# Performance work log

Measured on AMD Instinct MI355X. Metric: run time of the kernel, lower is better.

The kernel has to match this reference:

```python
import jax, jax.numpy as jnp
import numpy as np

D_MODEL = 1024
H = 16
D_K = D_MODEL // H
B = 2
S = 2048
NEG = -1000000000.0


def setup_inputs() -> dict:
    key = jax.random.key(0)
    ks = jax.random.split(key, 11)
    sc = 1.0 / np.sqrt(D_MODEL)
    inp = {
        "q": jax.random.normal(ks[0], (B, S, D_MODEL), jnp.float32),
        "k": jax.random.normal(ks[1], (B, S, D_MODEL), jnp.float32),
        "v": jax.random.normal(ks[2], (B, S, D_MODEL), jnp.float32),
        "mask": jnp.tril(jnp.ones((S, S), jnp.int32))[None, None, :, :],  # causal [1,1,S,S]
        "Wq": jax.random.normal(ks[3], (D_MODEL, D_MODEL), jnp.float32) * sc,
        "bq": jnp.zeros((D_MODEL,), jnp.float32),
        "Wk": jax.random.normal(ks[4], (D_MODEL, D_MODEL), jnp.float32) * sc,
        "bk": jnp.zeros((D_MODEL,), jnp.float32),
        "Wv": jax.random.normal(ks[5], (D_MODEL, D_MODEL), jnp.float32) * sc,
        "bv": jnp.zeros((D_MODEL,), jnp.float32),
        "Wo": jax.random.normal(ks[6], (D_MODEL, D_MODEL), jnp.float32) * sc,
        "bo": jnp.zeros((D_MODEL,), jnp.float32),
    }
    return inp


def reference(q, k, v, mask, Wq, bq, Wk, bk, Wv, bv, Wo, bo):
    # Linear projections (torch Linear: x @ W.T + b)
    query = q @ Wq.T + bq
    key_ = k @ Wk.T + bk
    value = v @ Wv.T + bv
    # [B,S,D] -> [B,H,S,Dk]
    def split_heads(x):
        return x.reshape(B, S, H, D_K).transpose(0, 2, 1, 3)
    query, key_, value = split_heads(query), split_heads(key_), split_heads(value)
    # scaled dot-product attention, scores [B,H,S,S]
    scores = jnp.einsum("bhqd,bhkd->bhqk", query, key_) / jnp.sqrt(
        jnp.asarray(D_K, query.dtype))
    scores = jnp.where(mask == 0, jnp.asarray(NEG, scores.dtype), scores)
    attn = jax.nn.softmax(scores, axis=-1)
    x = jnp.einsum("bhqk,bhkd->bhqd", attn, value)
    # merge heads [B,H,S,Dk] -> [B,S,D]
    x = x.transpose(0, 2, 1, 3).reshape(B, S, D_MODEL)
    return x @ Wo.T + bo
```

## Files before the change

kernel.cpp:

```cpp
#include <hip/hip_runtime.h>
#include <stdint.h>

#define D_MODEL 1024
#define NHEAD   16
#define DKH     64
#define NB      2
#define SSEQ    2048

typedef unsigned short u16;
typedef __bf16 bf16x8 __attribute__((ext_vector_type(8)));
typedef float  f32x4  __attribute__((ext_vector_type(4)));
typedef u16    u16x8  __attribute__((ext_vector_type(8)));

__device__ __forceinline__ u16 f2bf(float x) {
  union { float f; uint32_t u; } c; c.f = x;
  uint32_t r = c.u + 0x7FFFu + ((c.u >> 16) & 1u);
  return (u16)(r >> 16);
}

__device__ __forceinline__ void gload_lds16(const void* gsrc, void* ldsdst) {
  typedef const __attribute__((address_space(1))) uint32_t* gp_t;
  typedef __attribute__((address_space(3))) uint32_t* lp_t;
  gp_t g = reinterpret_cast<gp_t>(reinterpret_cast<uintptr_t>(gsrc));
  lp_t l = reinterpret_cast<lp_t>(reinterpret_cast<uintptr_t>(ldsdst));
  __builtin_amdgcn_global_load_lds(g, l, 16, 0, 0);
}

__device__ __forceinline__ f32x4 mfma16(bf16x8 a, bf16x8 b, f32x4 c) {
  return __builtin_amdgcn_mfma_f32_16x16x32_bf16(a, b, c, 0, 0, 0);
}

__device__ __forceinline__ bf16x8 lds_frag(const u16* tile, int row, int kelem) {
  int chunk = (kelem >> 3) ^ (row & 7);
  return *reinterpret_cast<const bf16x8*>(
      reinterpret_cast<const char*>(tile) + row * 128 + chunk * 16);
}

template<int NROWS>
__device__ __forceinline__ void stage_tile(const u16* __restrict__ g, int row0, int ldk,
                                           int k0, u16* ldsbase, int wid, int lane) {
  constexpr int CPW = NROWS / 32;
  #pragma unroll
  for (int i = 0; i < CPW; ++i) {
    int c = wid * CPW + i;
    int row = c * 8 + (lane >> 3);
    int cchunk = (lane & 7) ^ (lane >> 3);
    const u16* src = g + (size_t)(row0 + row) * ldk + k0 + cchunk * 8;
    gload_lds16(src, reinterpret_cast<char*>(ldsbase) + c * 1024);
  }
}

__global__ __launch_bounds__(256) void cast_kernel(
    const float* __restrict__ s0, const float* __restrict__ s1,
    const float* __restrict__ s2, const float* __restrict__ s3,
    u16* __restrict__ d0, u16* __restrict__ d1, u16* __restrict__ d2, u16* __restrict__ d3,
    int n8) {
  const int z = blockIdx.z;
  const float* s = (z == 0) ? s0 : (z == 1) ? s1 : (z == 2) ? s2 : s3;
  u16* d = (z == 0) ? d0 : (z == 1) ? d1 : (z == 2) ? d2 : d3;
  int i = blockIdx.x * 256 + threadIdx.x;
  if (i >= n8) return;
  float4 a = reinterpret_cast<const float4*>(s)[2 * i];
  float4 b = reinterpret_cast<const float4*>(s)[2 * i + 1];
  u16x8 o;
  o[0] = f2bf(a.x); o[1] = f2bf(a.y); o[2] = f2bf(a.z); o[3] = f2bf(a.w);
  o[4] = f2bf(b.x); o[5] = f2bf(b.y); o[6] = f2bf(b.z); o[7] = f2bf(b.w);
  reinterpret_cast<u16x8*>(d)[i] = o;
}

__device__ __forceinline__ void gemm_core(const u16* __restrict__ A, const u16* __restrict__ W,
                                          u16* ldsA, u16* ldsB, int brow, int bcol,
                                          f32x4 acc[4][4]) {
  const int tid = threadIdx.x;
  const int lane = tid & 63;
  const int wid = tid >> 6;
  const int wr = wid >> 1;
  const int wc = wid & 1;
  f32x4 z4 = {0.f, 0.f, 0.f, 0.f};
  #pragma unroll
  for (int i = 0; i < 4; ++i)
    #pragma unroll
    for (int j = 0; j < 4; ++j) acc[i][j] = z4;

  stage_tile<128>(A, brow, D_MODEL, 0, ldsA, wid, lane);
  stage_tile<128>(W, bcol, D_MODEL, 0, ldsB, wid, lane);
  __syncthreads();
  int buf = 0;
  const int KT = D_MODEL / 64;
  for (int kt = 0; kt < KT; ++kt) {
    if (kt + 1 < KT) {
      stage_tile<128>(A, brow, D_MODEL, (kt + 1) * 64, ldsA + (buf ^ 1) * 8192, wid, lane);
      stage_tile<128>(W, bcol, D_MODEL, (kt + 1) * 64, ldsB + (buf ^ 1) * 8192, wid, lane);
    }
    const u16* tA = ldsA + buf * 8192;
    const u16* tB = ldsB + buf * 8192;
    #pragma unroll
    for (int kk = 0; kk < 2; ++kk) {
      const int ke = kk * 32 + ((lane >> 4) << 3);
      bf16x8 af[4], bf[4];
      #pragma unroll
      for (int i = 0; i < 4; ++i) af[i] = lds_frag(tA, wr * 64 + i * 16 + (lane & 15), ke);
      #pragma unroll
      for (int j = 0; j < 4; ++j) bf[j] = lds_frag(tB, wc * 64 + j * 16 + (lane & 15), ke);
      #pragma unroll
      for (int i = 0; i < 4; ++i)
        #pragma unroll
        for (int j = 0; j < 4; ++j) acc[i][j] = mfma16(af[i], bf[j], acc[i][j]);
    }
    __syncthreads();
    buf ^= 1;
  }
}

__global__ __launch_bounds__(256, 2) void gemm_qkv(
    const u16* __restrict__ x0, const u16* __restrict__ x1, const u16* __restrict__ x2,
    const u16* __restrict__ w0, const u16* __restrict__ w1, const u16* __restrict__ w2,
    const float* __restrict__ b0, const float* __restrict__ b1, const float* __restrict__ b2,
    u16* __restrict__ o0, u16* __restrict__ o1, u16* __restrict__ o2) {
  __shared__ u16 ldsA[2 * 128 * 64];
  __shared__ u16 ldsB[2 * 128 * 64];
  const int z = blockIdx.z;
  const u16* X = (z == 0) ? x0 : (z == 1) ? x1 : x2;
  const u16* W = (z == 0) ? w0 : (z == 1) ? w1 : w2;
  const float* bias = (z == 0) ? b0 : (z == 1) ? b1 : b2;
  u16* O = (z == 0) ? o0 : (z == 1) ? o1 : o2;
  const float scale = (z == 0) ? 0.125f : 1.0f;
  const int brow = blockIdx.y * 128;
  const int bcol = blockIdx.x * 128;
  f32x4 acc[4][4];
  gemm_core(X, W, ldsA, ldsB, brow, bcol, acc);
  const int lane = threadIdx.x & 63;
  const int wid = threadIdx.x >> 6;
  const int wr = wid >> 1, wc = wid & 1;
  #pragma unroll
  for (int j = 0; j < 4; ++j) {
    const int n = bcol + wc * 64 + j * 16 + (lane & 15);
    const float bn = bias[n];
    const int h = n >> 6, d = n & 63;
    #pragma unroll
    for (int i = 0; i < 4; ++i)
      #pragma unroll
      for (int r = 0; r < 4; ++r) {
        const int m = brow + wr * 64 + i * 16 + ((lane >> 4) << 2) + r;
        const int bb = m >> 11, s = m & (SSEQ - 1);
        O[(((size_t)(bb * NHEAD + h) * SSEQ + s) << 6) + d] = f2bf((acc[i][j][r] + bn) * scale);
      }
  }
}

__global__ __launch_bounds__(256, 2) void gemm_out(const u16* __restrict__ A,
                                                   const u16* __restrict__ W,
                                                   const float* __restrict__ bias,
                                                   float* __restrict__ out) {
  __shared__ u16 ldsA[2 * 128 * 64];
  __shared__ u16 ldsB[2 * 128 * 64];
  const int brow = blockIdx.y * 128;
  const int bcol = blockIdx.x * 128;
  f32x4 acc[4][4];
  gemm_core(A, W, ldsA, ldsB, brow, bcol, acc);
  const int lane = threadIdx.x & 63;
  const int wid = threadIdx.x >> 6;
  const int wr = wid >> 1, wc = wid & 1;
  #pragma unroll
  for (int j = 0; j < 4; ++j) {
    const int n = bcol + wc * 64 + j * 16 + (lane & 15);
    const float bn = bias[n];
    #pragma unroll
    for (int i = 0; i < 4; ++i)
      #pragma unroll
      for (int r = 0; r < 4; ++r) {
        const int m = brow + wr * 64 + i * 16 + ((lane >> 4) << 2) + r;
        out[(size_t)m * D_MODEL + n] = acc[i][j][r] + bn;
      }
  }
}

__global__ __launch_bounds__(256) void transpose_v(const u16* __restrict__ V,
                                                   u16* __restrict__ Vt) {
  __shared__ u16 t[64][72];
  const int tid = threadIdx.x;
  const int bh = blockIdx.y;
  const int s0 = blockIdx.x * 64;
  const u16* Vb = V + ((size_t)bh * SSEQ + s0) * DKH;
  const int row = tid >> 2;
  const int cg = (tid & 3) * 16;
  uint4 a = *reinterpret_cast<const uint4*>(Vb + (size_t)row * DKH + cg);
  uint4 b = *reinterpret_cast<const uint4*>(Vb + (size_t)row * DKH + cg + 8);
  *reinterpret_cast<uint4*>(&t[row][cg]) = a;
  *reinterpret_cast<uint4*>(&t[row][cg + 8]) = b;
  __syncthreads();
  const int d = tid >> 2;
  const int sg = (tid & 3) * 16;
  u16 vals[16];
  #pragma unroll
  for (int j = 0; j < 16; ++j) vals[j] = t[sg + j][d];
  u16* dst = Vt + ((size_t)bh * DKH + d) * SSEQ + s0 + sg;
  *reinterpret_cast<uint4*>(dst) = *reinterpret_cast<uint4*>(&vals[0]);
  *reinterpret_cast<uint4*>(dst + 8) = *reinterpret_cast<uint4*>(&vals[8]);
}

__global__ __launch_bounds__(256, 2) void attn_kernel(const u16* __restrict__ Q,
                                                      const u16* __restrict__ K,
                                                      const u16* __restrict__ Vt,
                                                      u16* __restrict__ ctx) {
  __shared__ u16 ldsK[2 * 64 * 64];
  __shared__ u16 ldsV[2 * 64 * 64];
  __shared__ u16 ldsP[4 * 16 * 64];
  const int tid = threadIdx.x;
  const int lane = tid & 63;
  const int wid = tid >> 6;
  const int bh = blockIdx.y;
  const int q0 = blockIdx.x * 64;
  const u16* Kb = K + (size_t)bh * SSEQ * DKH;
  const u16* Vb = Vt + (size_t)bh * DKH * SSEQ;

  const u16* Qp = Q + ((size_t)bh * SSEQ + q0 + wid * 16 + (lane & 15)) * DKH + ((lane >> 4) << 3);
  bf16x8 qf0 = *reinterpret_cast<const bf16x8*>(Qp);
  bf16x8 qf1 = *reinterpret_cast<const bf16x8*>(Qp + 32);

  f32x4 z4 = {0.f, 0.f, 0.f, 0.f};
  f32x4 acc[4];
  #pragma unroll
  for (int j = 0; j < 4; ++j) acc[j] = z4;
  float mrow[4] = {-1e30f, -1e30f, -1e30f, -1e30f};
  float lrow[4] = {0.f, 0.f, 0.f, 0.f};

  const int nt = blockIdx.x + 1;
  stage_tile<64>(Kb, 0, DKH, 0, ldsK, wid, lane);
  stage_tile<64>(Vb, 0, SSEQ, 0, ldsV, wid, lane);
  __syncthreads();
  int buf = 0;
  for (int t = 0; t < nt; ++t) {
    if (t + 1 < nt) {
      stage_tile<64>(Kb, (t + 1) * 64, DKH, 0, ldsK + (buf ^ 1) * 4096, wid, lane);
      stage_tile<64>(Vb, 0, SSEQ, (t + 1) * 64, ldsV + (buf ^ 1) * 4096, wid, lane);
    }
    const u16* tK = ldsK + buf * 4096;
    const u16* tV = ldsV + buf * 4096;

    f32x4 sf[4];
    #pragma unroll
    for (int jk = 0; jk < 4; ++jk) {
      bf16x8 k0f = lds_frag(tK, jk * 16 + (lane & 15), (lane >> 4) << 3);
      bf16x8 k1f = lds_frag(tK, jk * 16 + (lane & 15), 32 + ((lane >> 4) << 3));
      f32x4 s = mfma16(qf0, k0f, z4);
      s = mfma16(qf1, k1f, s);
      sf[jk] = s;
    }
    if (t == (int)blockIdx.x) {
      #pragma unroll
      for (int jk = 0; jk < 4; ++jk)
        #pragma unroll
        for (int r = 0; r < 4; ++r) {
          int kv = t * 64 + jk * 16 + (lane & 15);
          int qrow = q0 + wid * 16 + ((lane >> 4) << 2) + r;
          if (kv > qrow) sf[jk][r] = -1e9f;
        }
    }
    float scl[4];
    #pragma unroll
    for (int r = 0; r < 4; ++r) {
      float mx = fmaxf(fmaxf(sf[0][r], sf[1][r]), fmaxf(sf[2][r], sf[3][r]));
      #pragma unroll
      for (int dd = 1; dd < 16; dd <<= 1) mx = fmaxf(mx, __shfl_xor(mx, dd));
      float mn = fmaxf(mrow[r], mx);
      scl[r] = __expf(mrow[r] - mn);
      mrow[r] = mn;
      lrow[r] *= scl[r];
    }
    #pragma unroll
    for (int j = 0; j < 4; ++j)
      #pragma unroll
      for (int r = 0; r < 4; ++r) acc[j][r] *= scl[r];

    u16* myP = ldsP + wid * 1024;
    float rsum[4] = {0.f, 0.f, 0.f, 0.f};
    #pragma unroll
    for (int jk = 0; jk < 4; ++jk)
      #pragma unroll
      for (int r = 0; r < 4; ++r) {
        float p = __expf(sf[jk][r] - mrow[r]);
        rsum[r] += p;
        int row = ((lane >> 4) << 2) + r;
        int col = jk * 16 + (lane & 15);
        int chunk = (col >> 3) ^ (row & 7);
        *reinterpret_cast<u16*>(reinterpret_cast<char*>(myP) + row * 128 + chunk * 16 +
                                (col & 7) * 2) = f2bf(p);
      }
    #pragma unroll
    for (int r = 0; r < 4; ++r) {
      float s = rsum[r];
      #pragma unroll
      for (int dd = 1; dd < 16; dd <<= 1) s += __shfl_xor(s, dd);
      lrow[r] += s;
    }
    #pragma unroll
    for (int c = 0; c < 2; ++c) {
      bf16x8 pf = lds_frag(myP, lane & 15, c * 32 + ((lane >> 4) << 3));
      #pragma unroll
      for (int j = 0; j < 4; ++j) {
        bf16x8 vf = lds_frag(tV, j * 16 + (lane & 15), c * 32 + ((lane >> 4) << 3));
        acc[j] = mfma16(pf, vf, acc[j]);
      }
    }
    __syncthreads();
    buf ^= 1;
  }
  float inv[4];
  #pragma unroll
  for (int r = 0; r < 4; ++r) inv[r] = 1.0f / lrow[r];
  const int b = bh >> 4, h = bh & 15;
  #pragma unroll
  for (int j = 0; j < 4; ++j)
    #pragma unroll
    for (int r = 0; r < 4; ++r) {
      int qrow = q0 + wid * 16 + ((lane >> 4) << 2) + r;
      int d = j * 16 + (lane & 15);
      ctx[((size_t)b * SSEQ + qrow) * D_MODEL + h * DKH + d] = f2bf(acc[j][r] * inv[r]);
    }
}

extern "C" void kernel_launch(void* const* d_in, const int* in_sizes, int n_in,
                              void* d_out, int out_size, void* d_ws, size_t ws_size,
                              hipStream_t stream) {
  const float* q  = (const float*)d_in[0];
  const float* k  = (const float*)d_in[1];
  const float* v  = (const float*)d_in[2];
  const float* Wq = (const float*)d_in[4];
  const float* bq = (const float*)d_in[5];
  const float* Wk = (const float*)d_in[6];
  const float* bk = (const float*)d_in[7];
  const float* Wv = (const float*)d_in[8];
  const float* bv = (const float*)d_in[9];
  const float* Wo = (const float*)d_in[10];
  const float* bo = (const float*)d_in[11];

  char* ws = (char*)d_ws;
  const size_t SZ_QKV = (size_t)NB * SSEQ * D_MODEL * 2;
  const size_t SZ_W   = (size_t)D_MODEL * D_MODEL * 2;
  u16* qb  = (u16*)(ws);
  u16* kb  = (u16*)(ws + SZ_QKV);
  u16* vb  = (u16*)(ws + 2 * SZ_QKV);
  u16* wqb = (u16*)(ws + 3 * SZ_QKV);
  u16* wkb = (u16*)(ws + 3 * SZ_QKV + SZ_W);
  u16* wvb = (u16*)(ws + 3 * SZ_QKV + 2 * SZ_W);
  u16* wob = (u16*)(ws + 3 * SZ_QKV + 3 * SZ_W);
  u16* Qh  = (u16*)(ws + 3 * SZ_QKV + 4 * SZ_W);
  u16* Kh  = (u16*)(ws + 4 * SZ_QKV + 4 * SZ_W);
  u16* Vh  = (u16*)(ws + 5 * SZ_QKV + 4 * SZ_W);
  u16* Vth = (u16*)(ws + 6 * SZ_QKV + 4 * SZ_W);
  u16* ctx = (u16*)(ws + 7 * SZ_QKV + 4 * SZ_W);

  cast_kernel<<<dim3(2048, 1, 3), 256, 0, stream>>>(
      q, k, v, nullptr, qb, kb, vb, nullptr, (NB * SSEQ * D_MODEL) / 8);
  cast_kernel<<<dim3(512, 1, 4), 256, 0, stream>>>(
      Wq, Wk, Wv, Wo, wqb, wkb, wvb, wob, (D_MODEL * D_MODEL) / 8);
  gemm_qkv<<<dim3(8, 32, 3), 256, 0, stream>>>(qb, kb, vb, wqb, wkb, wvb,
                                               bq, bk, bv, Qh, Kh, Vh);
  transpose_v<<<dim3(SSEQ / 64, NB * NHEAD), 256, 0, stream>>>(Vh, Vth);
  attn_kernel<<<dim3(SSEQ / 64, NB * NHEAD), 256, 0, stream>>>(Qh, Kh, Vth, ctx);
  gemm_out<<<dim3(8, 32), 256, 0, stream>>>(ctx, wob, bo, (float*)d_out);
}
```

Before: 293.1 us.

## Restructure attention into per-wave paired causal strips with direct register loads

The attention kernel now gives each wave an independent 16-row query strip and pairs strip p with strip 127-p so causal work is balanced across waves. K and V fragments are loaded straight from global memory into registers instead of being staged through double-buffered LDS, which removes the block-wide barriers. Blocks are remapped so several heads are interleaved across the grid. The change also adds s_setprio around the MFMA sections and drops the occupancy hint from the launch bounds of the GEMM and attention kernels. The cost is more global and L2 traffic, since each wave re-reads K/V itself with no sharing across the block.

```diff
diff --git a/kernel.cpp b/kernel.cpp
--- a/kernel.cpp
+++ b/kernel.cpp
@@ -102,17 +102,19 @@
       for (int i = 0; i < 4; ++i) af[i] = lds_frag(tA, wr * 64 + i * 16 + (lane & 15), ke);
       #pragma unroll
       for (int j = 0; j < 4; ++j) bf[j] = lds_frag(tB, wc * 64 + j * 16 + (lane & 15), ke);
+      __builtin_amdgcn_s_setprio(1);
       #pragma unroll
       for (int i = 0; i < 4; ++i)
         #pragma unroll
         for (int j = 0; j < 4; ++j) acc[i][j] = mfma16(af[i], bf[j], acc[i][j]);
+      __builtin_amdgcn_s_setprio(0);
     }
     __syncthreads();
     buf ^= 1;
   }
 }
 
-__global__ __launch_bounds__(256, 2) void gemm_qkv(
+__global__ __launch_bounds__(256) void gemm_qkv(
     const u16* __restrict__ x0, const u16* __restrict__ x1, const u16* __restrict__ x2,
     const u16* __restrict__ w0, const u16* __restrict__ w1, const u16* __restrict__ w2,
     const float* __restrict__ b0, const float* __restrict__ b1, const float* __restrict__ b2,
@@ -148,10 +150,10 @@
   }
 }
 
-__global__ __launch_bounds__(256, 2) void gemm_out(const u16* __restrict__ A,
-                                                   const u16* __restrict__ W,
-                                                   const float* __restrict__ bias,
-                                                   float* __restrict__ out) {
+__global__ __launch_bounds__(256) void gemm_out(const u16* __restrict__ A,
+                                                const u16* __restrict__ W,
+                                                const float* __restrict__ bias,
+                                                float* __restrict__ out) {
   __shared__ u16 ldsA[2 * 128 * 64];
   __shared__ u16 ldsB[2 * 128 * 64];
   const int brow = blockIdx.y * 128;
@@ -199,61 +201,61 @@
   *reinterpret_cast<uint4*>(dst + 8) = *reinterpret_cast<uint4*>(&vals[8]);
 }
 
-__global__ __launch_bounds__(256, 2) void attn_kernel(const u16* __restrict__ Q,
-                                                      const u16* __restrict__ K,
-                                                      const u16* __restrict__ Vt,
-                                                      u16* __restrict__ ctx) {
-  __shared__ u16 ldsK[2 * 64 * 64];
-  __shared__ u16 ldsV[2 * 64 * 64];
-  __shared__ u16 ldsP[4 * 16 * 64];
-  const int tid = threadIdx.x;
-  const int lane = tid & 63;
-  const int wid = tid >> 6;
-  const int bh = blockIdx.y;
-  const int q0 = blockIdx.x * 64;
-  const u16* Kb = K + (size_t)bh * SSEQ * DKH;
-  const u16* Vb = Vt + (size_t)bh * DKH * SSEQ;
-
-  const u16* Qp = Q + ((size_t)bh * SSEQ + q0 + wid * 16 + (lane & 15)) * DKH + ((lane >> 4) << 3);
+__device__ __forceinline__ void attn_strip(const u16* __restrict__ Qb,
+                                           const u16* __restrict__ Kb,
+                                           const u16* __restrict__ Vb,
+                                           u16* __restrict__ ctxb,
+                                           u16* myP, int strip, int lane) {
+  const int g = lane >> 4;
+  const int q0 = strip * 16;
+  const int nt = (strip >> 2) + 1;
+  const u16* Qp = Qb + (size_t)(q0 + (lane & 15)) * DKH + (g << 3);
   bf16x8 qf0 = *reinterpret_cast<const bf16x8*>(Qp);
   bf16x8 qf1 = *reinterpret_cast<const bf16x8*>(Qp + 32);
 
   f32x4 z4 = {0.f, 0.f, 0.f, 0.f};
-  f32x4 acc[4];
-  #pragma unroll
-  for (int j = 0; j < 4; ++j) acc[j] = z4;
+  f32x4 acc[4] = {z4, z4, z4, z4};
   float mrow[4] = {-1e30f, -1e30f, -1e30f, -1e30f};
   float lrow[4] = {0.f, 0.f, 0.f, 0.f};
 
-  const int nt = blockIdx.x + 1;
-  stage_tile<64>(Kb, 0, DKH, 0, ldsK, wid, lane);
-  stage_tile<64>(Vb, 0, SSEQ, 0, ldsV, wid, lane);
-  __syncthreads();
-  int buf = 0;
+  bf16x8 kf[8], vf[8];
+  #pragma unroll
+  for (int jk = 0; jk < 4; ++jk)
+    #pragma unroll
+    for (int c = 0; c < 2; ++c)
+      kf[jk * 2 + c] = *reinterpret_cast<const bf16x8*>(
+          Kb + (size_t)(jk * 16 + (lane & 15)) * DKH + c * 32 + (g << 3));
+
   for (int t = 0; t < nt; ++t) {
+    #pragma unroll
+    for (int j = 0; j < 4; ++j)
+      #pragma unroll
+      for (int c = 0; c < 2; ++c)
+        vf[j * 2 + c] = *reinterpret_cast<const bf16x8*>(
+            Vb + (size_t)(j * 16 + (lane & 15)) * SSEQ + t * 64 + c * 32 + (g << 3));
+    f32x4 sf[4];
+    __builtin_amdgcn_s_setprio(1);
+    #pragma unroll
+    for (int jk = 0; jk < 4; ++jk) {
+      f32x4 s = mfma16(qf0, kf[jk * 2 + 0], z4);
+      sf[jk] = mfma16(qf1, kf[jk * 2 + 1], s);
+    }
+    __builtin_amdgcn_s_setprio(0);
     if (t + 1 < nt) {
-      stage_tile<64>(Kb, (t + 1) * 64, DKH, 0, ldsK + (buf ^ 1) * 4096, wid, lane);
-      stage_tile<64>(Vb, 0, SSEQ, (t + 1) * 64, ldsV + (buf ^ 1) * 4096, wid, lane);
-    }
-    const u16* tK = ldsK + buf * 4096;
-    const u16* tV = ldsV + buf * 4096;
-
-    f32x4 sf[4];
-    #pragma unroll
-    for (int jk = 0; jk < 4; ++jk) {
-      bf16x8 k0f = lds_frag(tK, jk * 16 + (lane & 15), (lane >> 4) << 3);
-      bf16x8 k1f = lds_frag(tK, jk * 16 + (lane & 15), 32 + ((lane >> 4) << 3));
-      f32x4 s = mfma16(qf0, k0f, z4);
-      s = mfma16(qf1, k1f, s);
-      sf[jk] = s;
-    }
-    if (t == (int)blockIdx.x) {
+      #pragma unroll
+      for (int jk = 0; jk < 4; ++jk)
+        #pragma unroll
+        for (int c = 0; c < 2; ++c)
+          kf[jk * 2 + c] = *reinterpret_cast<const bf16x8*>(
+              Kb + (size_t)((t + 1) * 64 + jk * 16 + (lane & 15)) * DKH + c * 32 + (g << 3));
+    }
+    if (t == nt - 1) {
       #pragma unroll
       for (int jk = 0; jk < 4; ++jk)
         #pragma unroll
         for (int r = 0; r < 4; ++r) {
           int kv = t * 64 + jk * 16 + (lane & 15);
-          int qrow = q0 + wid * 16 + ((lane >> 4) << 2) + r;
+          int qrow = q0 + g * 4 + r;
           if (kv > qrow) sf[jk][r] = -1e9f;
         }
     }
@@ -268,12 +270,6 @@
       mrow[r] = mn;
       lrow[r] *= scl[r];
     }
-    #pragma unroll
-    for (int j = 0; j < 4; ++j)
-      #pragma unroll
-      for (int r = 0; r < 4; ++r) acc[j][r] *= scl[r];
-
-    u16* myP = ldsP + wid * 1024;
     float rsum[4] = {0.f, 0.f, 0.f, 0.f};
     #pragma unroll
     for (int jk = 0; jk < 4; ++jk)
@@ -281,7 +277,7 @@
       for (int r = 0; r < 4; ++r) {
         float p = __expf(sf[jk][r] - mrow[r]);
         rsum[r] += p;
-        int row = ((lane >> 4) << 2) + r;
+        int row = g * 4 + r;
         int col = jk * 16 + (lane & 15);
         int chunk = (col >> 3) ^ (row & 7);
         *reinterpret_cast<u16*>(reinterpret_cast<char*>(myP) + row * 128 + chunk * 16 +
@@ -295,29 +291,48 @@
       lrow[r] += s;
     }
     #pragma unroll
+    for (int j = 0; j < 4; ++j)
+      #pragma unroll
+      for (int r = 0; r < 4; ++r) acc[j][r] *= scl[r];
+    #pragma unroll
     for (int c = 0; c < 2; ++c) {
-      bf16x8 pf = lds_frag(myP, lane & 15, c * 32 + ((lane >> 4) << 3));
-      #pragma unroll
-      for (int j = 0; j < 4; ++j) {
-        bf16x8 vf = lds_frag(tV, j * 16 + (lane & 15), c * 32 + ((lane >> 4) << 3));
-        acc[j] = mfma16(pf, vf, acc[j]);
-      }
-    }
-    __syncthreads();
-    buf ^= 1;
+      bf16x8 pf = lds_frag(myP, lane & 15, c * 32 + (g << 3));
+      __builtin_amdgcn_s_setprio(1);
+      #pragma unroll
+      for (int j = 0; j < 4; ++j) acc[j] = mfma16(pf, vf[j * 2 + c], acc[j]);
+      __builtin_amdgcn_s_setprio(0);
+    }
   }
   float inv[4];
   #pragma unroll
   for (int r = 0; r < 4; ++r) inv[r] = 1.0f / lrow[r];
-  const int b = bh >> 4, h = bh & 15;
   #pragma unroll
   for (int j = 0; j < 4; ++j)
     #pragma unroll
     for (int r = 0; r < 4; ++r) {
-      int qrow = q0 + wid * 16 + ((lane >> 4) << 2) + r;
+      int qrow = q0 + g * 4 + r;
       int d = j * 16 + (lane & 15);
-      ctx[((size_t)b * SSEQ + qrow) * D_MODEL + h * DKH + d] = f2bf(acc[j][r] * inv[r]);
-    }
+      ctxb[(size_t)qrow * D_MODEL + d] = f2bf(acc[j][r] * inv[r]);
+    }
+}
+
+__global__ __launch_bounds__(256) void attn_kernel(const u16* __restrict__ Q,
+                                                   const u16* __restrict__ K,
+                                                   const u16* __restrict__ Vt,
+                                                   u16* __restrict__ ctx) {
+  __shared__ u16 ldsP[4 * 16 * 64];
+  const int lane = threadIdx.x & 63;
+  const int wid = threadIdx.x >> 6;
+  const int L = blockIdx.x + 16 * blockIdx.y;
+  const int bh = ((L & 7) << 2) | ((L >> 3) & 3);
+  const int p = (((L >> 5) & 15) << 2) | wid;
+  const u16* Qb = Q + (size_t)bh * SSEQ * DKH;
+  const u16* Kb = K + (size_t)bh * SSEQ * DKH;
+  const u16* Vb = Vt + (size_t)bh * DKH * SSEQ;
+  u16* ctxb = ctx + (size_t)(bh >> 4) * SSEQ * D_MODEL + (bh & 15) * DKH;
+  u16* myP = ldsP + wid * 1024;
+  attn_strip(Qb, Kb, Vb, ctxb, myP, 127 - p, lane);
+  attn_strip(Qb, Kb, Vb, ctxb, myP, p, lane);
 }
 
 extern "C" void kernel_launch(void* const* d_in, const int* in_sizes, int n_in,
@@ -358,6 +373,6 @@
   gemm_qkv<<<dim3(8, 32, 3), 256, 0, stream>>>(qb, kb, vb, wqb, wkb, wvb,
                                                bq, bk, bv, Qh, Kh, Vh);
   transpose_v<<<dim3(SSEQ / 64, NB * NHEAD), 256, 0, stream>>>(Vh, Vth);
-  attn_kernel<<<dim3(SSEQ / 64, NB * NHEAD), 256, 0, stream>>>(Qh, Kh, Vth, ctx);
+  attn_kernel<<<dim3(16, 32), 256, 0, stream>>>(Qh, Kh, Vth, ctx);
   gemm_out<<<dim3(8, 32), 256, 0, stream>>>(ctx, wob, bo, (float*)d_out);
 }
```

Result: slower. 311.3 us (+6.2%).
